# Kernel tuning notes

Hardware: AMD Instinct MI355X
Metric: run time of the kernel (lower is better)

Reference implementation:

```python
import jax, jax.numpy as jnp
import numpy as np
import math

B, S, HID = 2, 2048, 1024
D = 64            # size_per_head
H = HID // D      # num heads = 16
ROT = 32          # rotary_hsize = size_per_head // 2


def _apply_rotary(qk, sinusoids):
    # qk: [B, S, H, D]; sinusoids: [B, 2, S, ROT]
    sin = sinusoids[:, 0, :, None, :]   # [B, S, 1, ROT]
    cos = sinusoids[:, 1, :, None, :]
    qk_rope = qk[..., :ROT]
    # torch.stack([-a[..., ::2], a[..., 1::2]], -1).reshape(a.shape)
    rot2 = jnp.stack([-qk_rope[..., ::2], qk_rope[..., 1::2]], axis=-1).reshape(qk_rope.shape)
    qk_rope = qk_rope * cos + rot2 * sin
    return jnp.concatenate([qk_rope, qk[..., ROT:]], axis=-1)


def setup_inputs() -> dict:
    key = jax.random.key(0)
    ks = jax.random.split(key, 8)
    sc = 1.0 / math.sqrt(HID)
    return {
        "x": jax.random.normal(ks[0], (B, S, HID), jnp.float32),
        "sinusoids": jax.random.normal(ks[1], (B, 2, S, ROT), jnp.float32),
        "attention_bias": jax.random.uniform(ks[2], (B, 1, S, S), jnp.float32),
        "Wq": jax.random.normal(ks[3], (HID, HID), jnp.float32) * sc,
        "bq": jnp.zeros((HID,), jnp.float32),
        "Wk": jax.random.normal(ks[4], (HID, HID), jnp.float32) * sc,
        "bk": jnp.zeros((HID,), jnp.float32),
        "Wv": jax.random.normal(ks[5], (HID, HID), jnp.float32) * sc,
        "bv": jnp.zeros((HID,), jnp.float32),
        "Wo": jax.random.normal(ks[6], (HID, HID), jnp.float32) * sc,
    }


def reference(x, sinusoids, attention_bias, Wq, bq, Wk, bk, Wv, bv, Wo):
    q = (x @ Wq + bq).reshape(B, S, H, D)
    k = (x @ Wk + bk).reshape(B, S, H, D)
    v = (x @ Wv + bv).reshape(B, S, H, D)
    # original concatenates q,k along the heads dim before rotary; since rotary
    # broadcasts over heads, applying it to each separately is identical math
    q = _apply_rotary(q, sinusoids)
    k = _apply_rotary(k, sinusoids)
    q = q / math.sqrt(D)
    scores = jnp.einsum('bqhd,bkhd->bhqk', q, k)          # [B,H,S,S]
    probs = jax.nn.softmax(scores, axis=-1)
    probs = probs * attention_bias                         # multiplicative bias AFTER softmax
    out = jnp.einsum('bhqk,bkhd->bqhd', probs, v)          # [B,S,H,D]
    out = out.reshape(B, S, HID)
    return out @ Wo
```

## Files before the change

kernel.cpp:

```cpp
#include <hip/hip_runtime.h>
#include <hip/hip_bf16.h>
#include <math.h>

#define B_   2
#define S_   2048
#define HID_ 1024
#define D_   64
#define H_   16
#define ROT_ 32
#define M_   (B_*S_)

typedef __attribute__((ext_vector_type(4))) short  short4v;
typedef __attribute__((ext_vector_type(8))) short  short8;
typedef __attribute__((ext_vector_type(4))) float  floatx4;
typedef __attribute__((ext_vector_type(16))) float floatx16;

__device__ __forceinline__ float bf2f(unsigned short u) {
  unsigned int x = ((unsigned int)u) << 16;
  return __builtin_bit_cast(float, x);
}
__device__ __forceinline__ unsigned short f2bf(float f) {
  unsigned int x = __builtin_bit_cast(unsigned int, f);
  x += 0x7fffu + ((x >> 16) & 1u);
  return (unsigned short)(x >> 16);
}
__device__ __forceinline__ float exp2a(float x) {
  float r; asm volatile("v_exp_f32 %0, %1\n\ts_nop 0" : "=v"(r) : "v"(x)); return r;
}
__device__ __forceinline__ float rcpa(float x) {
  float r; asm volatile("v_rcp_f32 %0, %1\n\ts_nop 0" : "=v"(r) : "v"(x)); return r;
}
__device__ __forceinline__ void gload_lds16(const unsigned short* g, unsigned short* l) {
  __builtin_amdgcn_global_load_lds(
      (const __attribute__((address_space(1))) unsigned int*)g,
      (__attribute__((address_space(3))) unsigned int*)l, 16, 0, 0);
}

__global__ void cast_bf16(const float* __restrict__ in, unsigned short* __restrict__ out) {
  int i = (blockIdx.x * 256 + threadIdx.x) * 4;
  floatx4 v = *(const floatx4*)(in + i);
  unsigned short o[4];
  o[0] = f2bf(v[0]); o[1] = f2bf(v[1]); o[2] = f2bf(v[2]); o[3] = f2bf(v[3]);
  *(unsigned long long*)(out + i) = *(unsigned long long*)o;
}

__global__ void transW(const float* __restrict__ W0, const float* __restrict__ W1,
                       const float* __restrict__ W2, const float* __restrict__ W3,
                       unsigned short* __restrict__ T0, unsigned short* __restrict__ T1,
                       unsigned short* __restrict__ T2, unsigned short* __restrict__ T3) {
  const float* W; unsigned short* T;
  int z = blockIdx.z;
  if (z == 0)      { W = W0; T = T0; }
  else if (z == 1) { W = W1; T = T1; }
  else if (z == 2) { W = W2; T = T2; }
  else             { W = W3; T = T3; }
  __shared__ float tile[32][33];
  int bx = blockIdx.x * 32, by = blockIdx.y * 32;
  int tx = threadIdx.x, ty = threadIdx.y;
  #pragma unroll
  for (int j = 0; j < 4; j++)
    tile[ty + j*8][tx] = W[(size_t)(by + ty + j*8) * HID_ + bx + tx];
  __syncthreads();
  #pragma unroll
  for (int j = 0; j < 4; j++)
    T[(size_t)(bx + ty + j*8) * HID_ + by + tx] = f2bf(tile[tx][ty + j*8]);
}

template <int MODE>
__global__ __launch_bounds__(256) void gemm_bt(
    const unsigned short* __restrict__ A,
    const unsigned short* __restrict__ Bt0, const unsigned short* __restrict__ Bt1,
    const unsigned short* __restrict__ Bt2,
    const float* __restrict__ bias0, const float* __restrict__ bias1,
    const float* __restrict__ bias2,
    void* __restrict__ out0, void* __restrict__ out1, void* __restrict__ out2,
    const float* __restrict__ sins, float sc0)
{
  const unsigned short* Bt; const float* bias; void* Out; float sc;
  if (blockIdx.z == 0)      { Bt = Bt0; bias = bias0; Out = out0; sc = sc0; }
  else if (blockIdx.z == 1) { Bt = Bt1; bias = bias1; Out = out1; sc = 1.f; }
  else                      { Bt = Bt2; bias = bias2; Out = out2; sc = 1.f; }
  const int K = HID_, N = HID_;
  int m0 = blockIdx.y * 128, n0 = blockIdx.x * 128;
  __shared__ alignas(16) unsigned short sA[128 * 32];
  __shared__ alignas(16) unsigned short sB[128 * 32];
  int t = threadIdx.x;
  int lane = t & 63, wave = t >> 6;
  int quad = lane >> 4, l16 = lane & 15;
  int wr = wave >> 1, wc = wave & 1;

  int srow = (lane >> 2), scol = (lane & 3) * 8;
  const unsigned short* gA0 = A  + (size_t)(m0 + wave*32 +  0 + srow) * K + scol;
  const unsigned short* gA1 = A  + (size_t)(m0 + wave*32 + 16 + srow) * K + scol;
  const unsigned short* gB0 = Bt + (size_t)(n0 + wave*32 +  0 + srow) * K + scol;
  const unsigned short* gB1 = Bt + (size_t)(n0 + wave*32 + 16 + srow) * K + scol;
  unsigned short* lA0 = sA + (wave*32 +  0) * 32;
  unsigned short* lA1 = sA + (wave*32 + 16) * 32;
  unsigned short* lB0 = sB + (wave*32 +  0) * 32;
  unsigned short* lB1 = sB + (wave*32 + 16) * 32;

  floatx4 acc[4][4];
  #pragma unroll
  for (int i = 0; i < 4; i++)
    #pragma unroll
    for (int j = 0; j < 4; j++)
      acc[i][j] = (floatx4){0.f, 0.f, 0.f, 0.f};

  for (int k0 = 0; k0 < K; k0 += 32) {
    gload_lds16(gA0 + k0, lA0);
    gload_lds16(gA1 + k0, lA1);
    gload_lds16(gB0 + k0, lB0);
    gload_lds16(gB1 + k0, lB1);
    __syncthreads();
    short8 af[4], bf[4];
    #pragma unroll
    for (int i = 0; i < 4; i++) {
      af[i] = *(const short8*)(sA + (wr * 64 + i * 16 + l16) * 32 + quad * 8);
      bf[i] = *(const short8*)(sB + (wc * 64 + i * 16 + l16) * 32 + quad * 8);
    }
    #pragma unroll
    for (int i = 0; i < 4; i++)
      #pragma unroll
      for (int j = 0; j < 4; j++)
        acc[i][j] = __builtin_amdgcn_mfma_f32_16x16x32_bf16(af[i], bf[j], acc[i][j], 0, 0, 0);
    __syncthreads();
  }

  #pragma unroll
  for (int i = 0; i < 4; i++) {
    int mbase = m0 + wr * 64 + i * 16 + quad * 4;
    #pragma unroll
    for (int j = 0; j < 4; j++) {
      int n = n0 + wc * 64 + j * 16 + l16;
      float bv = bias ? bias[n] : 0.f;
      if (MODE == 1) {
        #pragma unroll
        for (int r = 0; r < 4; r++)
          ((float*)Out)[(size_t)(mbase + r) * N + n] = acc[i][j][r] + bv;
      } else if (blockIdx.z == 2) {
        int bb = mbase >> 11, ss = mbase & 2047;
        int hh = n >> 6, dd = n & 63;
        unsigned short pk[4];
        #pragma unroll
        for (int r = 0; r < 4; r++) pk[r] = f2bf(acc[i][j][r] + bv);
        *(unsigned long long*)((unsigned short*)Out +
            (((size_t)(bb * H_ + hh) * D_ + dd) * S_ + ss)) = *(unsigned long long*)pk;
      } else if (j < 2) {
        int jh = j * 16 + l16;
        #pragma unroll
        for (int r = 0; r < 4; r++) {
          int row = mbase + r, bb = row >> 11, ss = row & 2047;
          float sn = sins[((size_t)(bb * 2 + 0) * S_ + ss) * ROT_ + jh];
          float cs = sins[((size_t)(bb * 2 + 1) * S_ + ss) * ROT_ + jh];
          float f = (jh & 1) ? (cs + sn) : (cs - sn);
          ((unsigned short*)Out)[(size_t)row * N + n] = f2bf((acc[i][j][r] + bv) * f * sc);
        }
      } else {
        #pragma unroll
        for (int r = 0; r < 4; r++)
          ((unsigned short*)Out)[(size_t)(mbase + r) * N + n] = f2bf((acc[i][j][r] + bv) * sc);
      }
    }
  }
}

__global__ __launch_bounds__(256) void attn(
    const unsigned short* __restrict__ Q, const unsigned short* __restrict__ Kb,
    const unsigned short* __restrict__ Vt, const float* __restrict__ bias,
    unsigned short* __restrict__ Out)
{
  int b = blockIdx.z, h = blockIdx.y;
  int t = threadIdx.x;
  int lane = t & 63, wave = t >> 6;
  int l32 = lane & 31, hl = lane >> 5;
  int q0 = blockIdx.x * 128 + wave * 32;
  const int RS = H_ * D_;

  __shared__ alignas(16) unsigned short sK[2][64 * 72];
  __shared__ alignas(16) unsigned short sV[2][64 * 72];

  const unsigned short* Qbase = Q + ((size_t)(b * S_) * H_ + h) * D_;
  const unsigned short* Kbase = Kb + ((size_t)(b * S_) * H_ + h) * D_;
  const unsigned short* Vbase = Vt + ((size_t)(b * H_) + h) * D_ * S_;

  short8 qf[4];
  {
    const unsigned short* qp = Qbase + (size_t)(q0 + l32) * RS + 8 * hl;
    qf[0] = *(const short8*)(qp);
    qf[1] = *(const short8*)(qp + 16);
    qf[2] = *(const short8*)(qp + 32);
    qf[3] = *(const short8*)(qp + 48);
  }

  int srow = t >> 2, sq = t & 3;
  const unsigned short* gK = Kbase + (size_t)srow * RS + sq * 16;
  const unsigned short* gV = Vbase + (size_t)srow * S_ + sq * 16;
  const int wOff = srow * 72 + sq * 16;

  const float* bp = bias + (size_t)b * S_ * S_ + (size_t)(q0 + l32) * S_ + 4 * hl;

  float l_run = 0.f;
  floatx16 o0, o1;
  #pragma unroll
  for (int r = 0; r < 16; r++) { o0[r] = 0.f; o1[r] = 0.f; }

  floatx4 kp[2], vp[2];
  kp[0] = *(const floatx4*)(gK);     kp[1] = *(const floatx4*)(gK + 8);
  vp[0] = *(const floatx4*)(gV);     vp[1] = *(const floatx4*)(gV + 8);
  *(floatx4*)(&sK[0][wOff])     = kp[0];
  *(floatx4*)(&sK[0][wOff + 8]) = kp[1];
  *(floatx4*)(&sV[0][wOff])     = vp[0];
  *(floatx4*)(&sV[0][wOff + 8]) = vp[1];
  kp[0] = *(const floatx4*)(gK + (size_t)64 * RS);
  kp[1] = *(const floatx4*)(gK + (size_t)64 * RS + 8);
  vp[0] = *(const floatx4*)(gV + 64);
  vp[1] = *(const floatx4*)(gV + 64 + 8);

  for (int it = 0; it < S_ / 64; ++it) {
    int cur = it & 1, nxt = cur ^ 1;
    int k0 = it * 64;
    __syncthreads();

    if (it < S_ / 64 - 1) {
      *(floatx4*)(&sK[nxt][wOff])     = kp[0];
      *(floatx4*)(&sK[nxt][wOff + 8]) = kp[1];
      *(floatx4*)(&sV[nxt][wOff])     = vp[0];
      *(floatx4*)(&sV[nxt][wOff + 8]) = vp[1];
    }
    {
      int k2 = ((it + 2) & (S_ / 64 - 1)) * 64;
      kp[0] = *(const floatx4*)(gK + (size_t)k2 * RS);
      kp[1] = *(const floatx4*)(gK + (size_t)k2 * RS + 8);
      vp[0] = *(const floatx4*)(gV + k2);
      vp[1] = *(const floatx4*)(gV + k2 + 8);
    }

    floatx4 bl[8];
    #pragma unroll
    for (int cc = 0; cc < 2; cc++)
      #pragma unroll
      for (int rg = 0; rg < 4; rg++)
        bl[cc * 4 + rg] = *(const floatx4*)(bp + k0 + cc * 32 + 8 * rg);

    floatx16 st[2];
    #pragma unroll
    for (int cc = 0; cc < 2; cc++) {
      floatx16 s;
      #pragma unroll
      for (int r = 0; r < 16; r++) s[r] = 0.f;
      #pragma unroll
      for (int ks = 0; ks < 4; ks++) {
        short8 kf = *(const short8*)(&sK[cur][(cc * 32 + l32) * 72 + 16 * ks + 8 * hl]);
        s = __builtin_amdgcn_mfma_f32_32x32x16_bf16(kf, qf[ks], s, 0, 0, 0);
      }
      st[cc] = s;
    }

    short4v pf[2][4];
    #pragma unroll
    for (int cc = 0; cc < 2; cc++)
      #pragma unroll
      for (int rg = 0; rg < 4; rg++) {
        short4v pk;
        #pragma unroll
        for (int j = 0; j < 4; j++) {
          float p = exp2a(st[cc][rg * 4 + j]);
          l_run += p;
          pk[j] = (short)f2bf(p * bl[cc * 4 + rg][j]);
        }
        pf[cc][rg] = pk;
      }

    #pragma unroll
    for (int cc = 0; cc < 2; cc++)
      #pragma unroll
      for (int g = 0; g < 4; g++) {
        int kcol = cc * 32 + 8 * g + 4 * hl;
        short4v vf0 = *(const short4v*)(&sV[cur][(l32)      * 72 + kcol]);
        short4v vf1 = *(const short4v*)(&sV[cur][(32 + l32) * 72 + kcol]);
        o0 = __builtin_amdgcn_mfma_f32_32x32x8bf16_1k(pf[cc][g], vf0, o0, 0, 0, 0);
        o1 = __builtin_amdgcn_mfma_f32_32x32x8bf16_1k(pf[cc][g], vf1, o1, 0, 0, 0);
      }
  }

  float linv = rcpa(l_run + __shfl_xor(l_run, 32));

  #pragma unroll
  for (int r = 0; r < 16; r++) {
    int q_local = (r & 3) + 8 * (r >> 2) + 4 * hl;
    float sc = __shfl(linv, q_local);
    size_t base = ((size_t)(b * S_ + q0 + q_local) * H_ + h) * D_;
    Out[base + l32]      = f2bf(o0[r] * sc);
    Out[base + 32 + l32] = f2bf(o1[r] * sc);
  }
}

extern "C" void kernel_launch(void* const* d_in, const int* in_sizes, int n_in,
                              void* d_out, int out_size, void* d_ws, size_t ws_size,
                              hipStream_t stream) {
  (void)in_sizes; (void)n_in; (void)out_size; (void)ws_size;
  const float* x    = (const float*)d_in[0];
  const float* sins = (const float*)d_in[1];
  const float* ab   = (const float*)d_in[2];
  const float* Wq   = (const float*)d_in[3];
  const float* bq   = (const float*)d_in[4];
  const float* Wk   = (const float*)d_in[5];
  const float* bk   = (const float*)d_in[6];
  const float* Wv   = (const float*)d_in[7];
  const float* bv   = (const float*)d_in[8];
  const float* Wo   = (const float*)d_in[9];
  float* out = (float*)d_out;
  char* ws = (char*)d_ws;

  unsigned short* xb  = (unsigned short*)(ws);
  unsigned short* Wqt = (unsigned short*)(ws + ((size_t) 8 << 20));
  unsigned short* Wkt = (unsigned short*)(ws + ((size_t)10 << 20));
  unsigned short* Wvt = (unsigned short*)(ws + ((size_t)12 << 20));
  unsigned short* Wot = (unsigned short*)(ws + ((size_t)14 << 20));
  unsigned short* Qb  = (unsigned short*)(ws + ((size_t)16 << 20));
  unsigned short* Kb  = (unsigned short*)(ws + ((size_t)24 << 20));
  unsigned short* Vtb = (unsigned short*)(ws + ((size_t)32 << 20));
  unsigned short* Ab  = (unsigned short*)(ws + ((size_t)40 << 20));

  const float c1 = 0.125f * 1.44269504088896f;

  cast_bf16<<<dim3((M_ * HID_) / (256 * 4)), dim3(256), 0, stream>>>(x, xb);
  transW<<<dim3(32, 32, 4), dim3(32, 8), 0, stream>>>(Wq, Wk, Wv, Wo, Wqt, Wkt, Wvt, Wot);
  gemm_bt<0><<<dim3(8, 32, 3), dim3(256), 0, stream>>>(xb, Wqt, Wkt, Wvt, bq, bk, bv,
                                                       Qb, Kb, Vtb, sins, c1);
  attn<<<dim3(S_ / 128, H_, B_), dim3(256), 0, stream>>>(Qb, Kb, Vtb, ab, Ab);
  gemm_bt<1><<<dim3(8, 32, 1), dim3(256), 0, stream>>>(Ab, Wot, Wot, Wot,
                                                       nullptr, nullptr, nullptr,
                                                       out, out, out, sins, 1.f);
}
```

Before: 278.0 us.

## Split attention over key dimension with partial-sum combine kernel

Splits the attention key range into two halves, doubling the grid from 512 to 1024 blocks so more of the 256 CUs stay busy. Each split writes unnormalised fp32 partial outputs and row sums, and a new combine kernel adds them, normalises and writes bf16. Since the softmax has no max subtraction, the partials can simply be summed. The exp and bf16 packing also move to builtins with packed conversion. The cost is an extra kernel launch and fp32 partial traffic of about 16 MB.

```diff
diff --git a/kernel.cpp b/kernel.cpp
--- a/kernel.cpp
+++ b/kernel.cpp
@@ -9,6 +9,9 @@
 #define H_   16
 #define ROT_ 32
 #define M_   (B_*S_)
+#define NSPLIT 2
+#define KSPAN (S_ / NSPLIT)
+#define NT    (KSPAN / 64)
 
 typedef __attribute__((ext_vector_type(4))) short  short4v;
 typedef __attribute__((ext_vector_type(8))) short  short8;
@@ -24,11 +27,9 @@
   x += 0x7fffu + ((x >> 16) & 1u);
   return (unsigned short)(x >> 16);
 }
-__device__ __forceinline__ float exp2a(float x) {
-  float r; asm volatile("v_exp_f32 %0, %1\n\ts_nop 0" : "=v"(r) : "v"(x)); return r;
-}
-__device__ __forceinline__ float rcpa(float x) {
-  float r; asm volatile("v_rcp_f32 %0, %1\n\ts_nop 0" : "=v"(r) : "v"(x)); return r;
+__device__ __forceinline__ unsigned int pkbf(float a, float b) {
+  __hip_bfloat162 h = __float22bfloat162_rn(float2{a, b});
+  unsigned int u; __builtin_memcpy(&u, &h, 4); return u;
 }
 __device__ __forceinline__ void gload_lds16(const unsigned short* g, unsigned short* l) {
   __builtin_amdgcn_global_load_lds(
@@ -167,21 +168,26 @@
 __global__ __launch_bounds__(256) void attn(
     const unsigned short* __restrict__ Q, const unsigned short* __restrict__ Kb,
     const unsigned short* __restrict__ Vt, const float* __restrict__ bias,
-    unsigned short* __restrict__ Out)
+    float* __restrict__ Opart, float* __restrict__ Lpart)
 {
-  int b = blockIdx.z, h = blockIdx.y;
+  int z = blockIdx.z, b = z / NSPLIT, split = z % NSPLIT;
+  int h = blockIdx.y;
   int t = threadIdx.x;
   int lane = t & 63, wave = t >> 6;
   int l32 = lane & 31, hl = lane >> 5;
   int q0 = blockIdx.x * 128 + wave * 32;
+  int kbase = split * KSPAN;
   const int RS = H_ * D_;
+  const size_t pidx = ((size_t)z * H_ + h) * (S_ / 128) + blockIdx.x;
+  float* Oslab = Opart + pidx * (128 * 64);
+  float* Lslab = Lpart + pidx * 128;
 
   __shared__ alignas(16) unsigned short sK[2][64 * 72];
   __shared__ alignas(16) unsigned short sV[2][64 * 72];
 
   const unsigned short* Qbase = Q + ((size_t)(b * S_) * H_ + h) * D_;
-  const unsigned short* Kbase = Kb + ((size_t)(b * S_) * H_ + h) * D_;
-  const unsigned short* Vbase = Vt + ((size_t)(b * H_) + h) * D_ * S_;
+  const unsigned short* Kbase = Kb + ((size_t)(b * S_ + kbase) * H_ + h) * D_;
+  const unsigned short* Vbase = Vt + (((size_t)(b * H_) + h) * D_) * S_ + kbase;
 
   short8 qf[4];
   {
@@ -197,7 +203,7 @@
   const unsigned short* gV = Vbase + (size_t)srow * S_ + sq * 16;
   const int wOff = srow * 72 + sq * 16;
 
-  const float* bp = bias + (size_t)b * S_ * S_ + (size_t)(q0 + l32) * S_ + 4 * hl;
+  const float* bp = bias + (size_t)b * S_ * S_ + (size_t)(q0 + l32) * S_ + kbase + 4 * hl;
 
   float l_run = 0.f;
   floatx16 o0, o1;
@@ -216,19 +222,19 @@
   vp[0] = *(const floatx4*)(gV + 64);
   vp[1] = *(const floatx4*)(gV + 64 + 8);
 
-  for (int it = 0; it < S_ / 64; ++it) {
+  for (int it = 0; it < NT; ++it) {
     int cur = it & 1, nxt = cur ^ 1;
-    int k0 = it * 64;
+    int kt = it * 64;
     __syncthreads();
 
-    if (it < S_ / 64 - 1) {
+    if (it < NT - 1) {
       *(floatx4*)(&sK[nxt][wOff])     = kp[0];
       *(floatx4*)(&sK[nxt][wOff + 8]) = kp[1];
       *(floatx4*)(&sV[nxt][wOff])     = vp[0];
       *(floatx4*)(&sV[nxt][wOff + 8]) = vp[1];
     }
     {
-      int k2 = ((it + 2) & (S_ / 64 - 1)) * 64;
+      int k2 = ((it + 2) & (NT - 1)) * 64;
       kp[0] = *(const floatx4*)(gK + (size_t)k2 * RS);
       kp[1] = *(const floatx4*)(gK + (size_t)k2 * RS + 8);
       vp[0] = *(const floatx4*)(gV + k2);
@@ -240,7 +246,7 @@
     for (int cc = 0; cc < 2; cc++)
       #pragma unroll
       for (int rg = 0; rg < 4; rg++)
-        bl[cc * 4 + rg] = *(const floatx4*)(bp + k0 + cc * 32 + 8 * rg);
+        bl[cc * 4 + rg] = *(const floatx4*)(bp + kt + cc * 32 + 8 * rg);
 
     floatx16 st[2];
     #pragma unroll
@@ -261,14 +267,17 @@
     for (int cc = 0; cc < 2; cc++)
       #pragma unroll
       for (int rg = 0; rg < 4; rg++) {
-        short4v pk;
-        #pragma unroll
-        for (int j = 0; j < 4; j++) {
-          float p = exp2a(st[cc][rg * 4 + j]);
-          l_run += p;
-          pk[j] = (short)f2bf(p * bl[cc * 4 + rg][j]);
-        }
-        pf[cc][rg] = pk;
+        float p0 = __builtin_amdgcn_exp2f(st[cc][rg * 4 + 0]);
+        float p1 = __builtin_amdgcn_exp2f(st[cc][rg * 4 + 1]);
+        float p2 = __builtin_amdgcn_exp2f(st[cc][rg * 4 + 2]);
+        float p3 = __builtin_amdgcn_exp2f(st[cc][rg * 4 + 3]);
+        l_run += (p0 + p1) + (p2 + p3);
+        floatx4 bv = bl[cc * 4 + rg];
+        unsigned int lo = pkbf(p0 * bv[0], p1 * bv[1]);
+        unsigned int hi = pkbf(p2 * bv[2], p3 * bv[3]);
+        union { unsigned int u[2]; short4v s4; } u;
+        u.u[0] = lo; u.u[1] = hi;
+        pf[cc][rg] = u.s4;
       }
 
     #pragma unroll
@@ -283,15 +292,38 @@
       }
   }
 
-  float linv = rcpa(l_run + __shfl_xor(l_run, 32));
-
+  float lsum = l_run + __shfl_xor(l_run, 32);
+  if (hl == 0) Lslab[wave * 32 + l32] = lsum;
   #pragma unroll
   for (int r = 0; r < 16; r++) {
-    int q_local = (r & 3) + 8 * (r >> 2) + 4 * hl;
-    float sc = __shfl(linv, q_local);
-    size_t base = ((size_t)(b * S_ + q0 + q_local) * H_ + h) * D_;
-    Out[base + l32]      = f2bf(o0[r] * sc);
-    Out[base + 32 + l32] = f2bf(o1[r] * sc);
+    int q_local = wave * 32 + (r & 3) + 8 * (r >> 2) + 4 * hl;
+    Oslab[(size_t)q_local * 64 + l32]      = o0[r];
+    Oslab[(size_t)q_local * 64 + 32 + l32] = o1[r];
+  }
+}
+
+__global__ __launch_bounds__(256) void combine(
+    const float* __restrict__ Opart, const float* __restrict__ Lpart,
+    unsigned short* __restrict__ Ab)
+{
+  int qt = blockIdx.x, h = blockIdx.y, b = blockIdx.z;
+  int t = threadIdx.x;
+  int q = t >> 1, d0 = (t & 1) * 32;
+  size_t p0 = ((size_t)(b * NSPLIT + 0) * H_ + h) * (S_ / 128) + qt;
+  size_t p1 = ((size_t)(b * NSPLIT + 1) * H_ + h) * (S_ / 128) + qt;
+  float linv = __builtin_amdgcn_rcpf(Lpart[p0 * 128 + q] + Lpart[p1 * 128 + q]);
+  const float* O0 = Opart + p0 * (128 * 64) + (size_t)q * 64 + d0;
+  const float* O1 = Opart + p1 * (128 * 64) + (size_t)q * 64 + d0;
+  unsigned short* dst = Ab + ((size_t)(b * S_ + qt * 128 + q) * H_ + h) * D_ + d0;
+  #pragma unroll
+  for (int i = 0; i < 8; i++) {
+    floatx4 a = *(const floatx4*)(O0 + 4 * i);
+    floatx4 c = *(const floatx4*)(O1 + 4 * i);
+    a = a + c;
+    unsigned int w[2];
+    w[0] = pkbf(a[0] * linv, a[1] * linv);
+    w[1] = pkbf(a[2] * linv, a[3] * linv);
+    *(unsigned long long*)(dst + 4 * i) = *(unsigned long long*)w;
   }
 }
 
@@ -321,6 +353,8 @@
   unsigned short* Kb  = (unsigned short*)(ws + ((size_t)24 << 20));
   unsigned short* Vtb = (unsigned short*)(ws + ((size_t)32 << 20));
   unsigned short* Ab  = (unsigned short*)(ws + ((size_t)40 << 20));
+  float*          Opart = (float*)(ws + ((size_t)48 << 20));
+  float*          Lpart = (float*)(ws + ((size_t)80 << 20));
 
   const float c1 = 0.125f * 1.44269504088896f;
 
@@ -328,7 +362,9 @@
   transW<<<dim3(32, 32, 4), dim3(32, 8), 0, stream>>>(Wq, Wk, Wv, Wo, Wqt, Wkt, Wvt, Wot);
   gemm_bt<0><<<dim3(8, 32, 3), dim3(256), 0, stream>>>(xb, Wqt, Wkt, Wvt, bq, bk, bv,
                                                        Qb, Kb, Vtb, sins, c1);
-  attn<<<dim3(S_ / 128, H_, B_), dim3(256), 0, stream>>>(Qb, Kb, Vtb, ab, Ab);
+  attn<<<dim3(S_ / 128, H_, B_ * NSPLIT), dim3(256), 0, stream>>>(Qb, Kb, Vtb, ab,
+                                                                  Opart, Lpart);
+  combine<<<dim3(S_ / 128, H_, B_), dim3(256), 0, stream>>>(Opart, Lpart, Ab);
   gemm_bt<1><<<dim3(8, 32, 1), dim3(256), 0, stream>>>(Ab, Wot, Wot, Wot,
                                                        nullptr, nullptr, nullptr,
                                                        out, out, out, sins, 1.f);
```

Result: slower. 285.9 us (+2.8%).
